# Performance work log

Hardware: AMD Instinct MI355X
Metric: run time of the kernel (lower is better)

## Reference

```python
import jax, jax.numpy as jnp
import numpy as np

NEG = -9e15

def setup_inputs() -> dict:
    key = jax.random.key(0)
    k1, k2, k3, k4 = jax.random.split(key, 4)
    N, F_IN, F_OUT = 8192, 256, 256
    h = jax.random.normal(k1, (N, F_IN), dtype=jnp.float32)
    adj = jax.random.randint(k2, (N, N), 0, 2, dtype=jnp.int32)
    W = jax.random.normal(k3, (F_IN, F_OUT), dtype=jnp.float32) * (1.0 / np.sqrt(F_IN))
    a = jax.random.normal(k4, (2 * F_OUT,), dtype=jnp.float32) * (1.0 / np.sqrt(2 * F_OUT))
    return {"h": h, "adj": adj, "W": W, "a": a}

def reference(h, adj, W, a):
    # Wh: [N, F_out]
    Wh = h @ W
    F_OUT = Wh.shape[1]
    a1, a2 = a[:F_OUT], a[F_OUT:]
    # cat-based score decomposes: e_ij = leaky_relu(a1.Wh_i + a2.Wh_j)
    s1 = Wh @ a1  # [N]
    s2 = Wh @ a2  # [N]
    e = jax.nn.leaky_relu(s1[:, None] + s2[None, :], negative_slope=0.2)  # [N, N]
    e = jnp.where(adj > 0, e, NEG)
    attention = jax.nn.softmax(e, axis=-1)
    # dropout is identity in eval mode
    return attention @ Wh
```

## Files before the change

### kernel.cpp

```cpp
#include <hip/hip_runtime.h>

typedef short s8v  __attribute__((ext_vector_type(8)));
typedef float f4v  __attribute__((ext_vector_type(4)));
typedef int   v4i  __attribute__((ext_vector_type(4)));
typedef float v4f  __attribute__((ext_vector_type(4)));
typedef int   v2i  __attribute__((ext_vector_type(2)));

#define NNODES 8192
#define FDIM   256
#define NJC    2
#define JLEN   4096
#define TROWS  64
#define KSTEP  32
#define NSTEP  128

__device__ __forceinline__ unsigned short f2bf(float f) {
    unsigned int x = __builtin_bit_cast(unsigned int, f);
    x += 0x7fffu + ((x >> 16) & 1u);
    return (unsigned short)(x >> 16);
}
__device__ __forceinline__ int cvt_pk(float lo, float hi) {
    int r;
    asm("v_cvt_pk_bf16_f32 %0, %1, %2" : "=v"(r) : "v"(lo), "v"(hi));
    return r;
}

__device__ __forceinline__ void barrier_lds_only() {
    asm volatile("s_waitcnt lgkmcnt(0)" ::: "memory");
    __builtin_amdgcn_s_barrier();
    asm volatile("" ::: "memory");
}

__global__ __launch_bounds__(256) void prep_kernel(const float* __restrict__ W,
                                                   const float* __restrict__ a,
                                                   unsigned short* __restrict__ WT,
                                                   float* __restrict__ v1,
                                                   float* __restrict__ v2) {
    if (blockIdx.x < 256) {
        int idx = blockIdx.x * 256 + threadIdx.x;
        int r = idx >> 8, c = idx & 255;
        WT[c * 256 + r] = f2bf(W[r * 256 + c]);
    } else {
        __shared__ float r1[256], r2[256];
        int b = blockIdx.x - 256, n = threadIdx.x;
        float w = W[(size_t)b * FDIM + n];
        r1[n] = w * a[n];
        r2[n] = w * a[FDIM + n];
        __syncthreads();
        for (int off = 128; off > 0; off >>= 1) {
            if (n < off) { r1[n] += r1[n + off]; r2[n] += r2[n + off]; }
            __syncthreads();
        }
        if (n == 0) { v1[b] = r1[0]; v2[b] = r2[0]; }
    }
}

__global__ __launch_bounds__(128) void wh_kernel(
    const float* __restrict__ h, const unsigned short* __restrict__ WT,
    const float* __restrict__ v1, const float* __restrict__ v2,
    unsigned short* __restrict__ PB,
    float* __restrict__ s1, float* __restrict__ s2)
{
    __shared__ float v1_lds[FDIM], v2_lds[FDIM];
    int tid = threadIdx.x;
    v1_lds[tid] = v1[tid];       v1_lds[tid + 128] = v1[tid + 128];
    v2_lds[tid] = v2[tid];       v2_lds[tid + 128] = v2[tid + 128];
    __syncthreads();

    int w = tid >> 6, lane = tid & 63, q = lane >> 4, l15 = lane & 15;
    int i_base = blockIdx.x * 32 + w * 16;

    f4v acc[16] = {};
    float s1p = 0.f, s2p = 0.f;

    for (int k0 = 0; k0 < 256; k0 += 32) {
        const float* hp = h + (size_t)(i_base + l15) * FDIM + k0 + q * 8;
        f4v h0 = *(const f4v*)hp;
        f4v h1 = *(const f4v*)(hp + 4);
        union { v4i u; s8v s; } af;
        af.u[0] = cvt_pk(h0[0], h0[1]);
        af.u[1] = cvt_pk(h0[2], h0[3]);
        af.u[2] = cvt_pk(h1[0], h1[1]);
        af.u[3] = cvt_pk(h1[2], h1[3]);
#pragma unroll
        for (int j = 0; j < 4; ++j) {
            s1p += h0[j] * v1_lds[k0 + q * 8 + j] + h1[j] * v1_lds[k0 + q * 8 + 4 + j];
            s2p += h0[j] * v2_lds[k0 + q * 8 + j] + h1[j] * v2_lds[k0 + q * 8 + 4 + j];
        }
#pragma unroll
        for (int t = 0; t < 16; ++t) {
            s8v bf = *(const s8v*)(WT + (size_t)(t * 16 + l15) * FDIM + k0 + q * 8);
            acc[t] = __builtin_amdgcn_mfma_f32_16x16x32_bf16(af.s, bf, acc[t], 0, 0, 0);
        }
    }

    s1p += __shfl_xor(s1p, 16, 64);
    s1p += __shfl_xor(s1p, 32, 64);
    s2p += __shfl_xor(s2p, 16, 64);
    s2p += __shfl_xor(s2p, 32, 64);
    if (lane < 16) {
        s1[i_base + lane] = s1p;
        s2[i_base + lane] = s2p;
    }

#pragma unroll
    for (int t = 0; t < 16; ++t) {
        int i0 = i_base + q * 4;
        size_t a16 = (size_t)((i0 >> 5) * 16 + t) * 512
                   + l15 * 32 + ((i0 >> 3) & 3) * 8 + (i0 & 7);
        v2i pk;
        pk[0] = cvt_pk(acc[t][0], acc[t][1]);
        pk[1] = cvt_pk(acc[t][2], acc[t][3]);
        *(v2i*)(PB + a16) = pk;
    }
}

__global__ __launch_bounds__(512, 2) void attn_partial(
    const int* __restrict__ adj, const unsigned short* __restrict__ PB,
    const float* __restrict__ s1, const float* __restrict__ s2,
    float* __restrict__ Npart, float* __restrict__ dpart)
{
    __shared__ float s2_lds[JLEN];
    __shared__ unsigned short P_lds[2][TROWS * KSTEP];
    __shared__ float dsum_lds[TROWS][4];

    int tid = threadIdx.x;
    int jc = blockIdx.x & 1, rt = blockIdx.x >> 1;
    int j0 = jc * JLEN;

    ((v4f*)s2_lds)[tid]       = ((const v4f*)(s2 + j0))[tid];
    ((v4f*)s2_lds)[tid + 512] = ((const v4f*)(s2 + j0))[tid + 512];

    bool producer = (tid >= 256);

    int p = tid & 255, m = p >> 2, idx = p & 3;
    int woff = ((idx * 64 + m) * 8) ^ (idx * 16);
    float s1v = 0.f;
    const int* arow = adj + (size_t)(rt * TROWS + m) * NNODES + j0 + idx * 8;
    v4i a1_0 = {}, a1_1 = {}, a2_0 = {}, a2_1 = {}, a3_0 = {}, a3_1 = {};

    int g = tid >> 6, lane = tid & 63, q = lane >> 4, l15 = lane & 15;
    const unsigned short* pbb = PB + (size_t)(jc * NSTEP) * 16 * 512 + l15 * 32 + q * 8;
    f4v acc[4][4] = {};
    s8v bfA[4], bfB[4];
    float dsum = 0.f;

    __syncthreads();

    if (producer) {
        s1v = s1[rt * TROWS + m];
        v4i c0 = __builtin_nontemporal_load((const v4i*)(arow));
        v4i c1 = __builtin_nontemporal_load((const v4i*)(arow + 4));
        a1_0 = __builtin_nontemporal_load((const v4i*)(arow + 1 * KSTEP));
        a1_1 = __builtin_nontemporal_load((const v4i*)(arow + 1 * KSTEP + 4));
        a2_0 = __builtin_nontemporal_load((const v4i*)(arow + 2 * KSTEP));
        a2_1 = __builtin_nontemporal_load((const v4i*)(arow + 2 * KSTEP + 4));
        a3_0 = __builtin_nontemporal_load((const v4i*)(arow + 3 * KSTEP));
        a3_1 = __builtin_nontemporal_load((const v4i*)(arow + 3 * KSTEP + 4));
        v4f sA = *(const v4f*)&s2_lds[idx * 8];
        v4f sB = *(const v4f*)&s2_lds[idx * 8 + 4];
        float pa[4], pb_[4];
#pragma unroll
        for (int j = 0; j < 4; ++j) {
            float x = s1v + sA[j];
            pa[j] = (c0[j] > 0) ? __expf(fmaxf(x, 0.2f * x)) : 0.0f; dsum += pa[j];
            float x2 = s1v + sB[j];
            pb_[j] = (c1[j] > 0) ? __expf(fmaxf(x2, 0.2f * x2)) : 0.0f; dsum += pb_[j];
        }
        v4i pv;
        pv[0] = cvt_pk(pa[0], pa[1]);
        pv[1] = cvt_pk(pa[2], pa[3]);
        pv[2] = cvt_pk(pb_[0], pb_[1]);
        pv[3] = cvt_pk(pb_[2], pb_[3]);
        *(v4i*)&P_lds[0][woff] = pv;
    } else {
#pragma unroll
        for (int t = 0; t < 4; ++t)
            bfA[t] = *(const s8v*)(pbb + (size_t)(g * 4 + t) * 512);
    }
    barrier_lds_only();

#define STEP(S, BCUR, BNXT) do {                                              \
    if (!producer) {                                                          \
        int sn = ((S) + 1 < NSTEP) ? (S) + 1 : 0;                             \
        _Pragma("unroll")                                                     \
        for (int t = 0; t < 4; ++t)                                           \
            BNXT[t] = *(const s8v*)(pbb + (size_t)(sn * 16 + g * 4 + t) * 512);\
        const unsigned short* pbuf = P_lds[(S) & 1];                          \
        _Pragma("unroll")                                                     \
        for (int rh = 0; rh < 4; ++rh) {                                      \
            s8v af = *(const s8v*)&pbuf[((q * 64 + rh * 16 + l15) * 8) ^ (q * 16)]; \
            _Pragma("unroll")                                                 \
            for (int t = 0; t < 4; ++t)                                       \
                acc[rh][t] = __builtin_amdgcn_mfma_f32_16x16x32_bf16(af, BCUR[t], acc[rh][t], 0, 0, 0); \
        }                                                                     \
    } else {                                                                  \
        int kn = ((S) < NSTEP - 4) ? ((S) + 4) * KSTEP : 0;                   \
        v4i nx0 = __builtin_nontemporal_load((const v4i*)(arow + kn));        \
        v4i nx1 = __builtin_nontemporal_load((const v4i*)(arow + kn + 4));    \
        if ((S) < NSTEP - 1) {                                                \
            v4f sA = *(const v4f*)&s2_lds[((S) + 1) * KSTEP + idx * 8];       \
            v4f sB = *(const v4f*)&s2_lds[((S) + 1) * KSTEP + idx * 8 + 4];   \
            float pa[4], pb_[4];                                              \
            _Pragma("unroll")                                                 \
            for (int j = 0; j < 4; ++j) {                                     \
                float x = s1v + sA[j];                                        \
                pa[j] = (a1_0[j] > 0) ? __expf(fmaxf(x, 0.2f * x)) : 0.0f;    \
                dsum += pa[j];                                                \
                float x2 = s1v + sB[j];                                       \
                pb_[j] = (a1_1[j] > 0) ? __expf(fmaxf(x2, 0.2f * x2)) : 0.0f; \
                dsum += pb_[j];                                               \
            }                                                                 \
            v4i pv;                                                           \
            pv[0] = cvt_pk(pa[0], pa[1]);                                     \
            pv[1] = cvt_pk(pa[2], pa[3]);                                     \
            pv[2] = cvt_pk(pb_[0], pb_[1]);                                   \
            pv[3] = cvt_pk(pb_[2], pb_[3]);                                   \
            *(v4i*)&P_lds[((S) + 1) & 1][woff] = pv;                          \
        }                                                                     \
        a1_0 = a2_0; a1_1 = a2_1;                                             \
        a2_0 = a3_0; a2_1 = a3_1;                                             \
        a3_0 = nx0;  a3_1 = nx1;                                              \
    }                                                                         \
    barrier_lds_only();                                                       \
} while (0)

    for (int sb = 0; sb < NSTEP; sb += 2) {
        STEP(sb, bfA, bfB);
        STEP(sb + 1, bfB, bfA);
    }
#undef STEP

    if (producer) dsum_lds[m][idx] = dsum;
    __syncthreads();
    if (tid < TROWS) {
        float d = dsum_lds[tid][0] + dsum_lds[tid][1] + dsum_lds[tid][2] + dsum_lds[tid][3];
        dpart[jc * NNODES + rt * TROWS + tid] = d;
    }

    if (!producer) {
#pragma unroll
        for (int rh = 0; rh < 4; ++rh)
#pragma unroll
            for (int r = 0; r < 4; ++r) {
                int row = rh * 16 + q * 4 + r;
                float* base = Npart + ((size_t)(jc * NNODES) + rt * TROWS + row) * FDIM;
#pragma unroll
                for (int t = 0; t < 4; ++t)
                    __builtin_nontemporal_store(acc[rh][t][r], base + g * 64 + t * 16 + l15);
            }
    }
}

__global__ __launch_bounds__(256) void reduce_kernel(
    const float* __restrict__ Npart, const float* __restrict__ dpart,
    float* __restrict__ out)
{
    int i = blockIdx.x, n = threadIdx.x;
    float d = 0.f, acc = 0.f;
#pragma unroll
    for (int jc = 0; jc < NJC; ++jc) {
        d += dpart[jc * NNODES + i];
        acc += Npart[((size_t)(jc * NNODES) + i) * FDIM + n];
    }
    out[(size_t)i * FDIM + n] = acc / fmaxf(d, 1e-30f);
}

extern "C" void kernel_launch(void* const* d_in, const int* in_sizes, int n_in,
                              void* d_out, int out_size, void* d_ws, size_t ws_size,
                              hipStream_t stream) {
    const float* h   = (const float*)d_in[0];
    const int*   adj = (const int*)d_in[1];
    const float* W   = (const float*)d_in[2];
    const float* a   = (const float*)d_in[3];
    float* out = (float*)d_out;

    char* ws = (char*)d_ws;
    unsigned short* PB = (unsigned short*)ws;
    float* s1 = (float*)(ws + (4u << 20));
    float* s2 = (float*)(ws + (4u << 20) + (32u << 10));
    unsigned short* WT = (unsigned short*)(ws + (4u << 20) + (64u << 10));
    float* v1 = (float*)(ws + (4u << 20) + (192u << 10));
    float* v2 = (float*)(ws + (4u << 20) + (193u << 10));
    float* dpart = (float*)(ws + (5u << 20));
    float* Npart = (float*)(ws + (8u << 20));

    hipLaunchKernelGGL(prep_kernel, dim3(512), dim3(256), 0, stream, W, a, WT, v1, v2);
    hipLaunchKernelGGL(wh_kernel, dim3(256), dim3(128), 0, stream, h, WT, v1, v2, PB, s1, s2);
    hipLaunchKernelGGL(attn_partial, dim3(128 * NJC), dim3(512), 0, stream,
                       adj, PB, s1, s2, Npart, dpart);
    hipLaunchKernelGGL(reduce_kernel, dim3(NNODES), dim3(256), 0, stream, Npart, dpart, out);
}
```

Baseline: 462.0 us.

## Batch producer/consumer pipeline into 4-step phases with 8-deep LDS ring

Restructures the warp-specialized producer/consumer loop so each barrier covers a phase of four K-steps instead of one. The P tile buffer grows from 2 to 8 slots, and adj prefetch moves to phase-granular register arrays. The goal is to cut the number of block-wide barriers by four times and let each side work longer between syncs. In exchange it uses more LDS and more producer registers, which may reduce occupancy.

```diff
diff --git a/kernel.cpp b/kernel.cpp
--- a/kernel.cpp
+++ b/kernel.cpp
@@ -13,6 +13,8 @@
 #define TROWS  64
 #define KSTEP  32
 #define NSTEP  128
+#define PHLEN  4
+#define PHASES 32
 
 __device__ __forceinline__ unsigned short f2bf(float f) {
     unsigned int x = __builtin_bit_cast(unsigned int, f);
@@ -121,7 +123,7 @@
     float* __restrict__ Npart, float* __restrict__ dpart)
 {
     __shared__ float s2_lds[JLEN];
-    __shared__ unsigned short P_lds[2][TROWS * KSTEP];
+    __shared__ unsigned short P_lds[8][TROWS * KSTEP];
     __shared__ float dsum_lds[TROWS][4];
 
     int tid = threadIdx.x;
@@ -137,99 +139,90 @@
     int woff = ((idx * 64 + m) * 8) ^ (idx * 16);
     float s1v = 0.f;
     const int* arow = adj + (size_t)(rt * TROWS + m) * NNODES + j0 + idx * 8;
-    v4i a1_0 = {}, a1_1 = {}, a2_0 = {}, a2_1 = {}, a3_0 = {}, a3_1 = {};
+    v4i A0[PHLEN] = {}, A1[PHLEN] = {}, B0[PHLEN] = {}, B1[PHLEN] = {};
 
     int g = tid >> 6, lane = tid & 63, q = lane >> 4, l15 = lane & 15;
     const unsigned short* pbb = PB + (size_t)(jc * NSTEP) * 16 * 512 + l15 * 32 + q * 8;
     f4v acc[4][4] = {};
-    s8v bfA[4], bfB[4];
+    s8v bfr[2][4];
     float dsum = 0.f;
 
-    __syncthreads();
-
-    if (producer) {
-        s1v = s1[rt * TROWS + m];
-        v4i c0 = __builtin_nontemporal_load((const v4i*)(arow));
-        v4i c1 = __builtin_nontemporal_load((const v4i*)(arow + 4));
-        a1_0 = __builtin_nontemporal_load((const v4i*)(arow + 1 * KSTEP));
-        a1_1 = __builtin_nontemporal_load((const v4i*)(arow + 1 * KSTEP + 4));
-        a2_0 = __builtin_nontemporal_load((const v4i*)(arow + 2 * KSTEP));
-        a2_1 = __builtin_nontemporal_load((const v4i*)(arow + 2 * KSTEP + 4));
-        a3_0 = __builtin_nontemporal_load((const v4i*)(arow + 3 * KSTEP));
-        a3_1 = __builtin_nontemporal_load((const v4i*)(arow + 3 * KSTEP + 4));
-        v4f sA = *(const v4f*)&s2_lds[idx * 8];
-        v4f sB = *(const v4f*)&s2_lds[idx * 8 + 4];
-        float pa[4], pb_[4];
-#pragma unroll
-        for (int j = 0; j < 4; ++j) {
-            float x = s1v + sA[j];
-            pa[j] = (c0[j] > 0) ? __expf(fmaxf(x, 0.2f * x)) : 0.0f; dsum += pa[j];
-            float x2 = s1v + sB[j];
-            pb_[j] = (c1[j] > 0) ? __expf(fmaxf(x2, 0.2f * x2)) : 0.0f; dsum += pb_[j];
-        }
-        v4i pv;
-        pv[0] = cvt_pk(pa[0], pa[1]);
-        pv[1] = cvt_pk(pa[2], pa[3]);
-        pv[2] = cvt_pk(pb_[0], pb_[1]);
-        pv[3] = cvt_pk(pb_[2], pb_[3]);
-        *(v4i*)&P_lds[0][woff] = pv;
-    } else {
-#pragma unroll
-        for (int t = 0; t < 4; ++t)
-            bfA[t] = *(const s8v*)(pbb + (size_t)(g * 4 + t) * 512);
-    }
-    barrier_lds_only();
-
-#define STEP(S, BCUR, BNXT) do {                                              \
-    if (!producer) {                                                          \
-        int sn = ((S) + 1 < NSTEP) ? (S) + 1 : 0;                             \
+#define PPHASE(PH, AC0, AC1, AN0, AN1) do {                                   \
+    _Pragma("unroll")                                                         \
+    for (int u = 0; u < PHLEN; ++u) {                                         \
+        int sl = 4 * ((PH) + 2) + u;                                          \
+        int kn = (sl < NSTEP) ? sl * KSTEP : 0;                               \
+        AN0[u] = __builtin_nontemporal_load((const v4i*)(arow + kn));         \
+        AN1[u] = __builtin_nontemporal_load((const v4i*)(arow + kn + 4));     \
+    }                                                                         \
+    _Pragma("unroll")                                                         \
+    for (int u = 0; u < PHLEN; ++u) {                                         \
+        int sc = 4 * ((PH) + 1) + u;                                          \
+        if (sc < NSTEP) {                                                     \
+            v4f sA = *(const v4f*)&s2_lds[sc * KSTEP + idx * 8];              \
+            v4f sB = *(const v4f*)&s2_lds[sc * KSTEP + idx * 8 + 4];          \
+            float pa[4], pb_[4];                                              \
+            _Pragma("unroll")                                                 \
+            for (int j = 0; j < 4; ++j) {                                     \
+                float x = s1v + sA[j];                                        \
+                pa[j] = (AC0[u][j] > 0) ? __expf(fmaxf(x, 0.2f * x)) : 0.0f;  \
+                dsum += pa[j];                                                \
+                float x2 = s1v + sB[j];                                       \
+                pb_[j] = (AC1[u][j] > 0) ? __expf(fmaxf(x2, 0.2f * x2)) : 0.0f;\
+                dsum += pb_[j];                                               \
+            }                                                                 \
+            v4i pv;                                                           \
+            pv[0] = cvt_pk(pa[0], pa[1]);   pv[1] = cvt_pk(pa[2], pa[3]);     \
+            pv[2] = cvt_pk(pb_[0], pb_[1]); pv[3] = cvt_pk(pb_[2], pb_[3]);   \
+            *(v4i*)&P_lds[sc & 7][woff] = pv;                                 \
+        }                                                                     \
+    }                                                                         \
+} while (0)
+
+#define CPHASE(PH) do {                                                       \
+    _Pragma("unroll")                                                         \
+    for (int u = 0; u < PHLEN; ++u) {                                         \
+        int s = 4 * (PH) + u;                                                 \
+        int sn = (s + 1 < NSTEP) ? s + 1 : 0;                                 \
         _Pragma("unroll")                                                     \
         for (int t = 0; t < 4; ++t)                                           \
-            BNXT[t] = *(const s8v*)(pbb + (size_t)(sn * 16 + g * 4 + t) * 512);\
-        const unsigned short* pbuf = P_lds[(S) & 1];                          \
+            bfr[(u + 1) & 1][t] = *(const s8v*)(pbb + (size_t)(sn * 16 + g * 4 + t) * 512); \
+        const unsigned short* pbuf = &P_lds[s & 7][0];                        \
         _Pragma("unroll")                                                     \
         for (int rh = 0; rh < 4; ++rh) {                                      \
             s8v af = *(const s8v*)&pbuf[((q * 64 + rh * 16 + l15) * 8) ^ (q * 16)]; \
             _Pragma("unroll")                                                 \
             for (int t = 0; t < 4; ++t)                                       \
-                acc[rh][t] = __builtin_amdgcn_mfma_f32_16x16x32_bf16(af, BCUR[t], acc[rh][t], 0, 0, 0); \
+                acc[rh][t] = __builtin_amdgcn_mfma_f32_16x16x32_bf16(af, bfr[u & 1][t], acc[rh][t], 0, 0, 0); \
         }                                                                     \
-    } else {                                                                  \
-        int kn = ((S) < NSTEP - 4) ? ((S) + 4) * KSTEP : 0;                   \
-        v4i nx0 = __builtin_nontemporal_load((const v4i*)(arow + kn));        \
-        v4i nx1 = __builtin_nontemporal_load((const v4i*)(arow + kn + 4));    \
-        if ((S) < NSTEP - 1) {                                                \
-            v4f sA = *(const v4f*)&s2_lds[((S) + 1) * KSTEP + idx * 8];       \
-            v4f sB = *(const v4f*)&s2_lds[((S) + 1) * KSTEP + idx * 8 + 4];   \
-            float pa[4], pb_[4];                                              \
-            _Pragma("unroll")                                                 \
-            for (int j = 0; j < 4; ++j) {                                     \
-                float x = s1v + sA[j];                                        \
-                pa[j] = (a1_0[j] > 0) ? __expf(fmaxf(x, 0.2f * x)) : 0.0f;    \
-                dsum += pa[j];                                                \
-                float x2 = s1v + sB[j];                                       \
-                pb_[j] = (a1_1[j] > 0) ? __expf(fmaxf(x2, 0.2f * x2)) : 0.0f; \
-                dsum += pb_[j];                                               \
-            }                                                                 \
-            v4i pv;                                                           \
-            pv[0] = cvt_pk(pa[0], pa[1]);                                     \
-            pv[1] = cvt_pk(pa[2], pa[3]);                                     \
-            pv[2] = cvt_pk(pb_[0], pb_[1]);                                   \
-            pv[3] = cvt_pk(pb_[2], pb_[3]);                                   \
-            *(v4i*)&P_lds[((S) + 1) & 1][woff] = pv;                          \
-        }                                                                     \
-        a1_0 = a2_0; a1_1 = a2_1;                                             \
-        a2_0 = a3_0; a2_1 = a3_1;                                             \
-        a3_0 = nx0;  a3_1 = nx1;                                              \
     }                                                                         \
-    barrier_lds_only();                                                       \
 } while (0)
 
-    for (int sb = 0; sb < NSTEP; sb += 2) {
-        STEP(sb, bfA, bfB);
-        STEP(sb + 1, bfB, bfA);
-    }
-#undef STEP
+    if (producer) {
+        s1v = s1[rt * TROWS + m];
+#pragma unroll
+        for (int u = 0; u < PHLEN; ++u) {
+            A0[u] = __builtin_nontemporal_load((const v4i*)(arow + u * KSTEP));
+            A1[u] = __builtin_nontemporal_load((const v4i*)(arow + u * KSTEP + 4));
+        }
+    } else {
+#pragma unroll
+        for (int t = 0; t < 4; ++t)
+            bfr[0][t] = *(const s8v*)(pbb + (size_t)(g * 4 + t) * 512);
+    }
+    barrier_lds_only();
+
+    if (producer) PPHASE(-1, A0, A1, B0, B1);
+    barrier_lds_only();
+
+    for (int ph = 0; ph < PHASES; ph += 2) {
+        if (producer) PPHASE(ph, B0, B1, A0, A1); else CPHASE(ph);
+        barrier_lds_only();
+        if (producer) PPHASE(ph + 1, A0, A1, B0, B1); else CPHASE(ph + 1);
+        barrier_lds_only();
+    }
+#undef PPHASE
+#undef CPHASE
 
     if (producer) dsum_lds[m][idx] = dsum;
     __syncthreads();
```

Measured after the change: 467.3 us. Within noise of the previous version (+1.2%).
